# Kernel tuning notes

Measured on AMD Instinct MI355X. Metric: run time of the kernel, lower is better.

The kernel has to match this reference:

```python
import jax, jax.numpy as jnp
import numpy as np

HIDDEN = 2048
QK_DIM = 2048
NUM_HEADS = 16
HEAD_DIM = QK_DIM // NUM_HEADS  # 128; RoPE rotates this many dims per head
B, T = 4, 2048
EPS = 1e-5


def setup_inputs() -> dict:
    key = jax.random.key(0)
    ks = jax.random.split(key, 10)
    return {
        "q_state": jax.random.normal(ks[0], (B, T, HIDDEN), jnp.float32),
        "k_state": jax.random.normal(ks[1], (B, T, HIDDEN), jnp.float32),
        "v_state": jax.random.normal(ks[2], (B, T, HIDDEN), jnp.float32),
        # torch Linear weights: [out_features, in_features], no bias
        "Wq": jax.random.normal(ks[3], (QK_DIM, HIDDEN), jnp.float32) * 0.02,
        "Wk": jax.random.normal(ks[4], (QK_DIM, HIDDEN), jnp.float32) * 0.02,
        "Wv": jax.random.normal(ks[5], (HIDDEN, HIDDEN), jnp.float32) * 0.02,
        "negator": jnp.asarray(1.0, jnp.float32),
        "q_gamma": jnp.ones((2 * QK_DIM,), jnp.float32),
        "q_beta": jnp.zeros((2 * QK_DIM,), jnp.float32),
        "k_gamma": jnp.ones((2 * QK_DIM,), jnp.float32),
        "k_beta": jnp.zeros((2 * QK_DIM,), jnp.float32),
        "offset": 0,
    }


def _layer_norm(x, gamma, beta):
    mu = jnp.mean(x, axis=-1, keepdims=True)
    var = jnp.mean(jnp.square(x - mu), axis=-1, keepdims=True)
    return (x - mu) * jax.lax.rsqrt(var + EPS) * gamma + beta


def _split_heads(x, n_heads):
    b, t, d = x.shape
    return x.reshape(b, t, n_heads, d // n_heads).transpose(0, 2, 1, 3)  # b h t f


def _rotate_half(x):
    # interleaved pairs: (x1, x2) -> (-x2, x1)
    x2 = x.reshape(*x.shape[:-1], x.shape[-1] // 2, 2)
    return jnp.stack((-x2[..., 1], x2[..., 0]), axis=-1).reshape(x.shape)


def _apply_rope(x, offset, rot_dim):
    # x: [b, h, t, f]; rotate first rot_dim features, pass the rest through
    t = (jnp.arange(x.shape[-2]) + offset).astype(jnp.float32)
    inv_freq = 1.0 / (10000.0 ** (jnp.arange(0, rot_dim, 2, dtype=jnp.float32) / rot_dim))
    freqs = t[:, None] * inv_freq[None, :]           # [t, rot_dim/2]
    freqs = jnp.repeat(freqs, 2, axis=-1)            # [t, rot_dim] interleaved
    cos, sin = jnp.cos(freqs), jnp.sin(freqs)
    xl, xr = x[..., :rot_dim], x[..., rot_dim:]
    xl = xl * cos + _rotate_half(xl) * sin
    return jnp.concatenate([xl, xr], axis=-1)


def reference(q_state, k_state, v_state, Wq, Wk, Wv, negator,
              q_gamma, q_beta, k_gamma, k_beta, offset):
    q = jnp.einsum("btd,fd->btf", q_state, Wq)
    k = jnp.einsum("btd,fd->btf", k_state, Wk)
    v = jnp.einsum("btd,fd->btf", v_state, Wv)
    q = jnp.concatenate((q, negator - q), axis=-1)   # [b, t, 2*QK_DIM]
    k = jnp.concatenate((k, negator - k), axis=-1)
    q = _layer_norm(q, q_gamma, q_beta)
    k = _layer_norm(k, k_gamma, k_beta)
    q = _split_heads(q, NUM_HEADS)                   # [b, h, t, 2*HEAD_DIM]
    k = _split_heads(k, NUM_HEADS)
    v = _split_heads(v, NUM_HEADS)                   # [b, h, t, HIDDEN/h]
    q = _apply_rope(q, offset, HEAD_DIM)
    k = _apply_rope(k, offset, HEAD_DIM)
    return q, k, v
```

## Files before the change

kernel.cpp:

```cpp
#include <hip/hip_runtime.h>
#include <hip/hip_fp16.h>

#define TDIM 2048
#define BDIM 4
#define MROWS 8192
#define NDIM 2048
#define KDIM 2048
#define NH 16

typedef __attribute__((ext_vector_type(8))) _Float16 f16x8;
typedef __attribute__((ext_vector_type(4))) _Float16 f16x4;
typedef __attribute__((ext_vector_type(4))) float f32x4;

__device__ __forceinline__ void load16_to_lds(const _Float16* g, _Float16* l) {
  __builtin_amdgcn_global_load_lds((const __attribute__((address_space(1))) void*)g,
                                   (__attribute__((address_space(3))) void*)l,
                                   16, 0, 0);
}

__global__ __launch_bounds__(256) void cvt6_kernel(
    const float* __restrict__ s0, const float* __restrict__ s1,
    const float* __restrict__ s2, const float* __restrict__ s3,
    const float* __restrict__ s4, const float* __restrict__ s5,
    _Float16* __restrict__ d0, _Float16* __restrict__ d1,
    _Float16* __restrict__ d2, _Float16* __restrict__ d3,
    _Float16* __restrict__ d4, _Float16* __restrict__ d5) {
  const int z = blockIdx.z;
  const float* s; _Float16* d; int n;
  switch (z) {
    case 0: s = s0; d = d0; n = MROWS * KDIM; break;
    case 1: s = s1; d = d1; n = MROWS * KDIM; break;
    case 2: s = s2; d = d2; n = MROWS * KDIM; break;
    case 3: s = s3; d = d3; n = NDIM * KDIM; break;
    case 4: s = s4; d = d4; n = NDIM * KDIM; break;
    default: s = s5; d = d5; n = NDIM * KDIM; break;
  }
  const int n4 = n >> 2;
  const int stride = gridDim.x * blockDim.x;
  for (int i = blockIdx.x * blockDim.x + threadIdx.x; i < n4; i += stride) {
    float4 f = ((const float4*)s)[i];
    f16x4 h;
    h.x = (_Float16)f.x; h.y = (_Float16)f.y;
    h.z = (_Float16)f.z; h.w = (_Float16)f.w;
    ((f16x4*)d)[i] = h;
  }
}

__global__ __launch_bounds__(256) void gemm_kernel(
    const _Float16* __restrict__ A0, const _Float16* __restrict__ A1,
    const _Float16* __restrict__ A2,
    const _Float16* __restrict__ W0, const _Float16* __restrict__ W1,
    const _Float16* __restrict__ W2,
    _Float16* __restrict__ qraw, _Float16* __restrict__ kraw,
    float* __restrict__ vout) {
  __shared__ __align__(16) _Float16 As[128 * 32];
  __shared__ __align__(16) _Float16 Bs[128 * 32];

  const int z = blockIdx.z;
  const _Float16* __restrict__ A  = (z == 0) ? A0 : ((z == 1) ? A1 : A2);
  const _Float16* __restrict__ Wt = (z == 0) ? W0 : ((z == 1) ? W1 : W2);

  const int tid  = threadIdx.x;
  const int wave = tid >> 6;
  const int lane = tid & 63;
  const int m0 = blockIdx.y * 128;
  const int n0 = blockIdx.x * 128;

  f32x4 acc[4][4];
  const f32x4 z4 = {0.f, 0.f, 0.f, 0.f};
#pragma unroll
  for (int i = 0; i < 4; ++i)
#pragma unroll
    for (int j = 0; j < 4; ++j) acc[i][j] = z4;

  const int wm = (wave >> 1) * 64;
  const int wn = (wave & 1) * 64;
  const int m_in = lane & 15;
  const int kq = lane >> 4;

  const int ch0 = tid,        r0 = ch0 >> 2, c0 = ch0 & 3;
  const int ch1 = 256 + tid,  r1 = ch1 >> 2, c1 = ch1 & 3;
  const size_t gA0 = (size_t)(m0 + r0) * KDIM + c0 * 8;
  const size_t gA1 = (size_t)(m0 + r1) * KDIM + c1 * 8;
  const size_t gB0 = (size_t)(n0 + r0) * KDIM + c0 * 8;
  const size_t gB1 = (size_t)(n0 + r1) * KDIM + c1 * 8;
  _Float16* ldsA0 = &As[(wave * 64) * 8];
  _Float16* ldsA1 = &As[(256 + wave * 64) * 8];
  _Float16* ldsB0 = &Bs[(wave * 64) * 8];
  _Float16* ldsB1 = &Bs[(256 + wave * 64) * 8];

  for (int k0 = 0; k0 < KDIM; k0 += 32) {
    load16_to_lds(A + gA0 + k0, ldsA0);
    load16_to_lds(A + gA1 + k0, ldsA1);
    load16_to_lds(Wt + gB0 + k0, ldsB0);
    load16_to_lds(Wt + gB1 + k0, ldsB1);
    __syncthreads();

    f16x8 a[4], b[4];
#pragma unroll
    for (int mi = 0; mi < 4; ++mi)
      a[mi] = *(const f16x8*)&As[(wm + mi * 16 + m_in) * 32 + kq * 8];
#pragma unroll
    for (int ni = 0; ni < 4; ++ni)
      b[ni] = *(const f16x8*)&Bs[(wn + ni * 16 + m_in) * 32 + kq * 8];
#pragma unroll
    for (int mi = 0; mi < 4; ++mi)
#pragma unroll
      for (int ni = 0; ni < 4; ++ni)
        acc[mi][ni] = __builtin_amdgcn_mfma_f32_16x16x32_f16(a[mi], b[ni], acc[mi][ni], 0, 0, 0);
    __syncthreads();
  }

  const int rbase = kq * 4;
  if (z < 2) {
    _Float16* __restrict__ raw = (z == 0) ? qraw : kraw;
#pragma unroll
    for (int mi = 0; mi < 4; ++mi) {
      const int m = m0 + wm + mi * 16 + rbase;
#pragma unroll
      for (int ni = 0; ni < 4; ++ni) {
        const int n = n0 + wn + ni * 16 + m_in;
#pragma unroll
        for (int r = 0; r < 4; ++r)
          raw[(size_t)(m + r) * NDIM + n] = (_Float16)acc[mi][ni][r];
      }
    }
  } else {
#pragma unroll
    for (int mi = 0; mi < 4; ++mi) {
      const int mb = m0 + wm + mi * 16 + rbase;
#pragma unroll
      for (int ni = 0; ni < 4; ++ni) {
        const int n = n0 + wn + ni * 16 + m_in;
        const int h = n >> 7, dd = n & 127;
#pragma unroll
        for (int r = 0; r < 4; ++r) {
          const int m = mb + r;
          const int b = m >> 11, t = m & 2047;
          vout[(((size_t)(b * NH + h) * TDIM) + t) * 128 + dd] = acc[mi][ni][r];
        }
      }
    }
  }
}

__global__ __launch_bounds__(256) void ln_rope_kernel(
    const _Float16* __restrict__ qraw, const _Float16* __restrict__ kraw,
    const float* __restrict__ negator,
    const float* __restrict__ q_gamma, const float* __restrict__ q_beta,
    const float* __restrict__ k_gamma, const float* __restrict__ k_beta,
    const int* __restrict__ offset_p,
    float* __restrict__ out) {
  const int row = blockIdx.x;
  const int mat = blockIdx.y;
  const _Float16* __restrict__ raw = mat ? kraw : qraw;
  const float* __restrict__ gamma = mat ? k_gamma : q_gamma;
  const float* __restrict__ beta  = mat ? k_beta  : q_beta;
  float* __restrict__ outb = out + (size_t)mat * ((size_t)BDIM * NH * TDIM * 256);

  const float c = negator[0];
  const float mu = 0.5f * c;
  const int tid = threadIdx.x;

  __shared__ __align__(16) float vals[2048];
  __shared__ float wred[4];

  const int b = row >> 11, t = row & 2047;
  const float tpos = (float)(t + offset_p[0]);
  const int d = tid;

  float sv = 0.f, cv = 0.f;
  if (d < 128) {
    const int p = d >> 1;
    const float invf = exp2f(-(float)p * 0.20762050592854797f);
    sincosf(tpos * invf, &sv, &cv);
  }

  f16x8 hv = ((const f16x8*)(raw + (size_t)row * 2048))[tid];
  float v[8];
  float ss = 0.f;
#pragma unroll
  for (int j = 0; j < 8; ++j) {
    float x = (float)hv[j] - mu;
    v[j] = x;
    ss += x * x;
  }
  ((float4*)vals)[tid * 2 + 0] = make_float4(v[0], v[1], v[2], v[3]);
  ((float4*)vals)[tid * 2 + 1] = make_float4(v[4], v[5], v[6], v[7]);

#pragma unroll
  for (int o = 32; o > 0; o >>= 1) ss += __shfl_down(ss, o, 64);
  if ((tid & 63) == 0) wred[tid >> 6] = ss;
  __syncthreads();
  const float var = (wred[0] + wred[1] + wred[2] + wred[3]) * (1.0f / 2048.0f);
  const float rstd = rsqrtf(var + 1e-5f);

#pragma unroll
  for (int i = 0; i < 16; ++i) {
    const int g = i * 256 + tid;
    const float sgn = (g < 2048) ? 1.f : -1.f;
    const float y = sgn * vals[g & 2047] * rstd * gamma[g] + beta[g];
    float res;
    if (d < 128) {
      const int gp = g ^ 1;
      const float yp = sgn * vals[gp & 2047] * rstd * gamma[gp] + beta[gp];
      res = (d & 1) ? (y * cv + yp * sv) : (y * cv - yp * sv);
    } else {
      res = y;
    }
    outb[(((size_t)(b * NH + i) * TDIM) + t) * 256 + d] = res;
  }
}

extern "C" void kernel_launch(void* const* d_in, const int* in_sizes, int n_in,
                              void* d_out, int out_size, void* d_ws, size_t ws_size,
                              hipStream_t stream) {
  (void)in_sizes; (void)n_in; (void)out_size; (void)ws_size;
  const float* q_state = (const float*)d_in[0];
  const float* k_state = (const float*)d_in[1];
  const float* v_state = (const float*)d_in[2];
  const float* Wq = (const float*)d_in[3];
  const float* Wk = (const float*)d_in[4];
  const float* Wv = (const float*)d_in[5];
  const float* negator = (const float*)d_in[6];
  const float* q_gamma = (const float*)d_in[7];
  const float* q_beta  = (const float*)d_in[8];
  const float* k_gamma = (const float*)d_in[9];
  const float* k_beta  = (const float*)d_in[10];
  const int* offset    = (const int*)d_in[11];

  float* out = (float*)d_out;
  float* vout = out + (size_t)2 * BDIM * NH * TDIM * 256;

  _Float16* Aq   = (_Float16*)d_ws;
  _Float16* Ak   = Aq + (size_t)MROWS * KDIM;
  _Float16* Av   = Ak + (size_t)MROWS * KDIM;
  _Float16* Wq16 = Av + (size_t)MROWS * KDIM;
  _Float16* Wk16 = Wq16 + (size_t)NDIM * KDIM;
  _Float16* Wv16 = Wk16 + (size_t)NDIM * KDIM;
  _Float16* qraw = Wv16 + (size_t)NDIM * KDIM;
  _Float16* kraw = qraw + (size_t)MROWS * NDIM;

  cvt6_kernel<<<dim3(2048, 1, 6), dim3(256), 0, stream>>>(
      q_state, k_state, v_state, Wq, Wk, Wv, Aq, Ak, Av, Wq16, Wk16, Wv16);

  gemm_kernel<<<dim3(16, 64, 3), dim3(256), 0, stream>>>(
      Aq, Ak, Av, Wq16, Wk16, Wv16, qraw, kraw, vout);

  ln_rope_kernel<<<dim3(8192, 2), dim3(256), 0, stream>>>(
      qraw, kraw, negator, q_gamma, q_beta, k_gamma, k_beta, offset, out);
}
```

Baseline: 909.6 us.

## Restructure GEMM into 256x256 tiles with 4-stage LDS pipeline and swizzle

Rewrites the projection GEMM to use 512-thread blocks computing 256x256 output tiles. Global-to-LDS loads run through a 4-deep ring buffer with explicit vmcnt waits, so loads overlap MFMA compute instead of doing load-sync-compute-sync per k-step. LDS layout is XOR-swizzled to avoid bank conflicts, block order is remapped so blocks running together share tiles in L2, and s_setprio raises priority around the MFMAs. The larger per-wave accumulator tile (8x4) raises register pressure, and the 128 KB of LDS may limit occupancy.

```diff
diff --git a/kernel.cpp b/kernel.cpp
--- a/kernel.cpp
+++ b/kernel.cpp
@@ -17,6 +17,12 @@
                                    (__attribute__((address_space(3))) void*)l,
                                    16, 0, 0);
 }
+
+#define WAITBAR(N) do { \
+  asm volatile("s_waitcnt vmcnt(" #N ")" ::: "memory"); \
+  __builtin_amdgcn_s_barrier(); \
+  __builtin_amdgcn_sched_barrier(0); \
+} while (0)
 
 __global__ __launch_bounds__(256) void cvt6_kernel(
     const float* __restrict__ s0, const float* __restrict__ s1,
@@ -46,76 +52,110 @@
   }
 }
 
-__global__ __launch_bounds__(256) void gemm_kernel(
+__global__ __launch_bounds__(512, 2) void gemm_kernel(
     const _Float16* __restrict__ A0, const _Float16* __restrict__ A1,
     const _Float16* __restrict__ A2,
     const _Float16* __restrict__ W0, const _Float16* __restrict__ W1,
     const _Float16* __restrict__ W2,
     _Float16* __restrict__ qraw, _Float16* __restrict__ kraw,
     float* __restrict__ vout) {
-  __shared__ __align__(16) _Float16 As[128 * 32];
-  __shared__ __align__(16) _Float16 Bs[128 * 32];
-
-  const int z = blockIdx.z;
+  __shared__ __align__(16) _Float16 lds[4][2][8192];
+
+  int lin = (blockIdx.z * gridDim.y + blockIdx.y) * gridDim.x + blockIdx.x;
+  lin = (lin & 7) * 96 + (lin >> 3);
+  const int z  = lin >> 8;
+  const int ty = (lin >> 3) & 31;
+  const int tx = lin & 7;
+
   const _Float16* __restrict__ A  = (z == 0) ? A0 : ((z == 1) ? A1 : A2);
   const _Float16* __restrict__ Wt = (z == 0) ? W0 : ((z == 1) ? W1 : W2);
+  const int m0 = ty * 256;
+  const int n0 = tx * 256;
 
   const int tid  = threadIdx.x;
   const int wave = tid >> 6;
   const int lane = tid & 63;
-  const int m0 = blockIdx.y * 128;
-  const int n0 = blockIdx.x * 128;
-
-  f32x4 acc[4][4];
+  const int m_in = lane & 15;
+  const int kq   = lane >> 4;
+  const int wave_m = wave >> 2;
+  const int wave_n = wave & 3;
+
+  f32x4 acc[8][4];
   const f32x4 z4 = {0.f, 0.f, 0.f, 0.f};
 #pragma unroll
-  for (int i = 0; i < 4; ++i)
+  for (int i = 0; i < 8; ++i)
 #pragma unroll
     for (int j = 0; j < 4; ++j) acc[i][j] = z4;
 
-  const int wm = (wave >> 1) * 64;
-  const int wn = (wave & 1) * 64;
-  const int m_in = lane & 15;
-  const int kq = lane >> 4;
-
-  const int ch0 = tid,        r0 = ch0 >> 2, c0 = ch0 & 3;
-  const int ch1 = 256 + tid,  r1 = ch1 >> 2, c1 = ch1 & 3;
-  const size_t gA0 = (size_t)(m0 + r0) * KDIM + c0 * 8;
-  const size_t gA1 = (size_t)(m0 + r1) * KDIM + c1 * 8;
-  const size_t gB0 = (size_t)(n0 + r0) * KDIM + c0 * 8;
-  const size_t gB1 = (size_t)(n0 + r1) * KDIM + c1 * 8;
-  _Float16* ldsA0 = &As[(wave * 64) * 8];
-  _Float16* ldsA1 = &As[(256 + wave * 64) * 8];
-  _Float16* ldsB0 = &Bs[(wave * 64) * 8];
-  _Float16* ldsB1 = &Bs[(256 + wave * 64) * 8];
-
-  for (int k0 = 0; k0 < KDIM; k0 += 32) {
-    load16_to_lds(A + gA0 + k0, ldsA0);
-    load16_to_lds(A + gA1 + k0, ldsA1);
-    load16_to_lds(Wt + gB0 + k0, ldsB0);
-    load16_to_lds(Wt + gB1 + k0, ldsB1);
-    __syncthreads();
-
-    f16x8 a[4], b[4];
-#pragma unroll
-    for (int mi = 0; mi < 4; ++mi)
-      a[mi] = *(const f16x8*)&As[(wm + mi * 16 + m_in) * 32 + kq * 8];
-#pragma unroll
-    for (int ni = 0; ni < 4; ++ni)
-      b[ni] = *(const f16x8*)&Bs[(wn + ni * 16 + m_in) * 32 + kq * 8];
-#pragma unroll
-    for (int mi = 0; mi < 4; ++mi)
+  const int P0 = tid * 16;
+  const int P1 = (512 + tid) * 16;
+  const int L0 = P0 ^ (((P0 >> 7) & 3) << 4);
+  const int L1 = P1 ^ (((P1 >> 7) & 3) << 4);
+  const _Float16* srcA0 = A  + (size_t)(m0 + (L0 >> 6)) * KDIM + ((L0 & 63) >> 1);
+  const _Float16* srcA1 = A  + (size_t)(m0 + (L1 >> 6)) * KDIM + ((L1 & 63) >> 1);
+  const _Float16* srcB0 = Wt + (size_t)(n0 + (L0 >> 6)) * KDIM + ((L0 & 63) >> 1);
+  const _Float16* srcB1 = Wt + (size_t)(n0 + (L1 >> 6)) * KDIM + ((L1 & 63) >> 1);
+  const int dst0 = (wave * 64) * 8;
+  const int dst1 = (512 + wave * 64) * 8;
+
+  int offA[8], offB[4];
+#pragma unroll
+  for (int mi = 0; mi < 8; ++mi) {
+    const int r = wave_m * 128 + mi * 16 + m_in;
+    offA[mi] = r * 64 + ((kq ^ ((r >> 1) & 3)) << 4);
+  }
+#pragma unroll
+  for (int ni = 0; ni < 4; ++ni) {
+    const int r = wave_n * 64 + ni * 16 + m_in;
+    offB[ni] = r * 64 + ((kq ^ ((r >> 1) & 3)) << 4);
+  }
+
+  auto stage = [&](int kt) {
+    _Float16* base = &lds[kt & 3][0][0];
+    const int ko = kt * 32;
+    load16_to_lds(srcA0 + ko, base + dst0);
+    load16_to_lds(srcA1 + ko, base + dst1);
+    load16_to_lds(srcB0 + ko, base + 8192 + dst0);
+    load16_to_lds(srcB1 + ko, base + 8192 + dst1);
+  };
+
+  auto compute = [&](int kt) {
+    const char* Ab = (const char*)&lds[kt & 3][0][0];
+    const char* Bb = (const char*)&lds[kt & 3][1][0];
+    f16x8 a[8], b[4];
+#pragma unroll
+    for (int mi = 0; mi < 8; ++mi) a[mi] = *(const f16x8*)(Ab + offA[mi]);
+#pragma unroll
+    for (int ni = 0; ni < 4; ++ni) b[ni] = *(const f16x8*)(Bb + offB[ni]);
+    __builtin_amdgcn_s_setprio(1);
+#pragma unroll
+    for (int mi = 0; mi < 8; ++mi)
 #pragma unroll
       for (int ni = 0; ni < 4; ++ni)
         acc[mi][ni] = __builtin_amdgcn_mfma_f32_16x16x32_f16(a[mi], b[ni], acc[mi][ni], 0, 0, 0);
-    __syncthreads();
-  }
+    __builtin_amdgcn_s_setprio(0);
+  };
+
+  stage(0); stage(1); stage(2);
+  WAITBAR(8);
+
+#pragma unroll 1
+  for (int kt = 0; kt < KDIM / 32 - 3; ++kt) {
+    stage(kt + 3);
+    compute(kt);
+    WAITBAR(8);
+  }
+  compute(KDIM / 32 - 3); WAITBAR(4);
+  compute(KDIM / 32 - 2); WAITBAR(0);
+  compute(KDIM / 32 - 1);
 
   const int rbase = kq * 4;
+  const int wm = wave_m * 128;
+  const int wn = wave_n * 64;
   if (z < 2) {
     _Float16* __restrict__ raw = (z == 0) ? qraw : kraw;
 #pragma unroll
-    for (int mi = 0; mi < 4; ++mi) {
+    for (int mi = 0; mi < 8; ++mi) {
       const int m = m0 + wm + mi * 16 + rbase;
 #pragma unroll
       for (int ni = 0; ni < 4; ++ni) {
@@ -127,7 +167,7 @@
     }
   } else {
 #pragma unroll
-    for (int mi = 0; mi < 4; ++mi) {
+    for (int mi = 0; mi < 8; ++mi) {
       const int mb = m0 + wm + mi * 16 + rbase;
 #pragma unroll
       for (int ni = 0; ni < 4; ++ni) {
@@ -244,7 +284,7 @@
   cvt6_kernel<<<dim3(2048, 1, 6), dim3(256), 0, stream>>>(
       q_state, k_state, v_state, Wq, Wk, Wv, Aq, Ak, Av, Wq16, Wk16, Wv16);
 
-  gemm_kernel<<<dim3(16, 64, 3), dim3(256), 0, stream>>>(
+  gemm_kernel<<<dim3(8, 32, 3), dim3(512), 0, stream>>>(
       Aq, Ak, Av, Wq16, Wk16, Wv16, qraw, kraw, vout);
 
   ln_rope_kernel<<<dim3(8192, 2), dim3(256), 0, stream>>>(
```

Result: faster. 761.0 us (-16.3%).
